# Optimization experiments

Measured on AMD Instinct MI355X. Metric: run time of the kernel, lower is better.

## Reference

```python
import jax, jax.numpy as jnp
import numpy as np

# Loss hyperparameters (from init_kwargs defaults)
ALPHA, BETA, GAMMA = 1.0, 2.0, 1.0
DAY_W, NIGHT_W = 2.0, 0.5
PEAK_WIN_W, PEAK_WIN = 3.0, 2
HIGH_POWER_W, POWER_PCT = 1.5, 0.75
HOURS = 24

B, S = 4096, 4032  # seq_len = 24 * 168 days


def setup_inputs() -> dict:
    key = jax.random.key(0)
    k1, k2 = jax.random.split(key)
    y_true = jax.random.uniform(k1, (B, S), dtype=jnp.float32)
    # predictions = truth + noise, clipped to be realistic power values
    y_pred = y_true + 0.1 * jax.random.normal(k2, (B, S), dtype=jnp.float32)
    return {"y_pred": y_pred, "y_true": y_true}


def _daily_peaks(y, day_mask):
    # y, day_mask: (B, D, H). Peaks restricted to daytime hours.
    masked = jnp.where(day_mask, y, jnp.float32(-1e9))
    times = jnp.argmax(masked, axis=-1)                                   # (B, D) int
    vals = jnp.take_along_axis(y, times[..., None], axis=-1)[..., 0]      # (B, D)
    return times, vals


def reference(y_pred, y_true):
    b, s = y_true.shape
    d = s // HOURS
    # default is_daytime: hour-of-day in [6, 20]
    hour = jnp.arange(HOURS, dtype=jnp.int32)
    day_hour_mask = (hour >= 6) & (hour <= 20)                            # (H,)
    is_daytime = jnp.broadcast_to(day_hour_mask[None, None, :], (b, d, HOURS))

    yt = y_true.reshape(b, d, HOURS)
    yp = y_pred.reshape(b, d, HOURS)

    true_times, true_peaks = _daily_peaks(yt, is_daytime)
    pred_times, pred_peaks = _daily_peaks(yp, is_daytime)
    peak_time_errors = (pred_times - true_times).astype(jnp.float32)      # (B, D)

    # --- step weights: day/night base, x PEAK_WIN_W in [peak-2, peak+2] ---
    base_w = jnp.where(is_daytime, jnp.float32(DAY_W), jnp.float32(NIGHT_W))  # (B,D,H)
    pt = true_times[..., None]                                            # (B,D,1)
    in_window = (hour[None, None, :] >= pt - PEAK_WIN) & (hour[None, None, :] <= pt + PEAK_WIN)
    step_w = base_w * jnp.where(in_window, jnp.float32(PEAK_WIN_W), jnp.float32(1.0))
    step_w = step_w.reshape(b, s)

    sq_err = (y_pred - y_true) ** 2
    L_overall = jnp.sum(sq_err * step_w) / jnp.sum(step_w)

    # --- peak magnitude loss with high-power sample weighting ---
    sample_avg_peaks = jnp.mean(true_peaks, axis=1)                       # (B,)
    thr = jnp.quantile(sample_avg_peaks, POWER_PCT)
    high = sample_avg_peaks > thr                                         # (B,) bool
    sample_w = jnp.where(high[:, None], jnp.float32(HIGH_POWER_W), jnp.float32(1.0))
    sample_w = jnp.broadcast_to(sample_w, true_peaks.shape)               # (B, D)
    peak_sq = (pred_peaks - true_peaks) ** 2
    L_peak_mag = jnp.sum(peak_sq * sample_w) / jnp.sum(sample_w)

    L_peak_timing = jnp.mean(jnp.abs(peak_time_errors) * 10.0)

    return ALPHA * L_overall + BETA * L_peak_mag + GAMMA * L_peak_timing
```

## Files before the change

kernel.cpp:

```cpp
#include <hip/hip_runtime.h>
#include <math.h>

#define S_LEN   4032
#define HOURS   24
#define DAYS    168
#define DAY_PAD 28
#define NB_MAX  4096


__device__ inline float block_reduce_f(float v, float* scratch, int tid) {
#pragma unroll
    for (int o = 32; o > 0; o >>= 1) v += __shfl_down(v, o, 64);
    if ((tid & 63) == 0) scratch[tid >> 6] = v;
    __syncthreads();
    float r = 0.f;
    if (tid == 0) r = scratch[0] + scratch[1] + scratch[2] + scratch[3];
    __syncthreads();
    return r;
}

__device__ inline double block_reduce_d(double v, double* scratch, int tid) {
#pragma unroll
    for (int o = 32; o > 0; o >>= 1) v += __shfl_down(v, o, 64);
    if ((tid & 63) == 0) scratch[tid >> 6] = v;
    __syncthreads();
    double r = 0.0;
    if (tid == 0) r = scratch[0] + scratch[1] + scratch[2] + scratch[3];
    __syncthreads();
    return r;
}


__global__ __launch_bounds__(256, 4) void day_kernel(
    const float* __restrict__ y_pred, const float* __restrict__ y_true,
    float* __restrict__ A, float* __restrict__ P,
    float* __restrict__ SEp, float* __restrict__ SWp, float* __restrict__ Tp)
{
    __shared__ float s_yt[DAYS * DAY_PAD];
    __shared__ float s_yp[DAYS * DAY_PAD];
    __shared__ float s_red[4];

    const int tid = threadIdx.x;
    const int b = blockIdx.x;
    const size_t base = (size_t)b * S_LEN;
    const float4* gp = (const float4*)(y_pred + base);
    const float4* gt = (const float4*)(y_true + base);

    for (int i = tid; i < S_LEN / 4; i += 256) {
        float4 vp = gp[i];
        float4 vt = gt[i];
        int f = i * 4;
        int d = f / HOURS;
        int off = f - d * HOURS;
        *(float4*)&s_yp[d * DAY_PAD + off] = vp;
        *(float4*)&s_yt[d * DAY_PAD + off] = vt;
    }
    __syncthreads();

    float tpeak = 0.f, psq = 0.f, se = 0.f, sw = 0.f, terr = 0.f;
    if (tid < DAYS) {
        const float4* rt = (const float4*)&s_yt[tid * DAY_PAD];
        const float4* rp = (const float4*)&s_yp[tid * DAY_PAD];
        float yt[HOURS];
#pragma unroll
        for (int j = 0; j < 6; ++j) {
            float4 q = rt[j];
            yt[j * 4 + 0] = q.x; yt[j * 4 + 1] = q.y;
            yt[j * 4 + 2] = q.z; yt[j * 4 + 3] = q.w;
        }
        float tbest = yt[6]; int tt = 6;
#pragma unroll
        for (int h = 7; h <= 20; ++h) {
            if (yt[h] > tbest) { tbest = yt[h]; tt = h; }
        }
        float pbest = -1e30f; int pt = 6;
#pragma unroll
        for (int j = 0; j < 6; ++j) {
            float4 q = rp[j];
            float pv[4] = {q.x, q.y, q.z, q.w};
#pragma unroll
            for (int k = 0; k < 4; ++k) {
                int h = j * 4 + k;
                float v = pv[k];
                bool day = (h >= 6) && (h <= 20);
                if (day && v > pbest) { pbest = v; pt = h; }
                float bw = day ? 2.0f : 0.5f;
                float w = bw * (((h >= tt - 2) && (h <= tt + 2)) ? 3.0f : 1.0f);
                float dd = v - yt[h];
                se += dd * dd * w;
                sw += w;
            }
        }
        tpeak = tbest;
        float dp = pbest - tbest;
        psq = dp * dp;
        terr = fabsf((float)(pt - tt));
    }

    float rA = block_reduce_f(tpeak, s_red, tid);
    float rP = block_reduce_f(psq,   s_red, tid);
    float rE = block_reduce_f(se,    s_red, tid);
    float rW = block_reduce_f(sw,    s_red, tid);
    float rT = block_reduce_f(terr,  s_red, tid);
    if (tid == 0) {
        A[b]   = rA * (1.0f / (float)DAYS);
        P[b]   = rP;
        SEp[b] = rE;
        SWp[b] = rW;
        Tp[b]  = rT;
    }
}


__global__ __launch_bounds__(256) void finalize_kernel(
    const float* __restrict__ A, const float* __restrict__ P,
    const float* __restrict__ SEp, const float* __restrict__ SWp,
    const float* __restrict__ Tp, float* __restrict__ out, int nB)
{
    __shared__ unsigned s_keys[NB_MAX];
    __shared__ unsigned s_hist[256];
    __shared__ unsigned s_wtot[4];
    __shared__ unsigned s_sel, s_srem;
    __shared__ double s_dred[4];

    const int tid = threadIdx.x;

    for (int i = tid; i < nB; i += 256) {
        unsigned u = __float_as_uint(A[i]);
        s_keys[i] = (u & 0x80000000u) ? ~u : (u | 0x80000000u);
    }
    __syncthreads();

    double pos = 0.75 * (double)(nB - 1);
    int lo = (int)pos;
    double frac = pos - (double)lo;
    int hi = (lo + 1 < nB) ? lo + 1 : lo;
    int ranks[2] = {lo, hi};
    float qv[2];

    for (int sidx = 0; sidx < 2; ++sidx) {
        int rem = ranks[sidx];
        unsigned prefix = 0;
        for (int shift = 24; shift >= 0; shift -= 8) {
            s_hist[tid] = 0;
            __syncthreads();
            unsigned maskAbove = (shift == 24) ? 0u : (0xFFFFFFFFu << (shift + 8));
            for (int i = tid; i < nB; i += 256) {
                unsigned k = s_keys[i];
                if ((k & maskAbove) == prefix)
                    atomicAdd(&s_hist[(k >> shift) & 0xFFu], 1u);
            }
            __syncthreads();
            unsigned c = s_hist[tid];
            unsigned x = c;
#pragma unroll
            for (int o = 1; o < 64; o <<= 1) {
                unsigned y = __shfl_up(x, o, 64);
                if ((tid & 63) >= o) x += y;
            }
            if ((tid & 63) == 63) s_wtot[tid >> 6] = x;
            __syncthreads();
            unsigned woff = 0;
            for (int w2 = 0; w2 < (tid >> 6); ++w2) woff += s_wtot[w2];
            unsigned incl = woff + x;
            unsigned excl = incl - c;
            if ((unsigned)rem >= excl && (unsigned)rem < incl) {
                s_sel = (unsigned)tid;
                s_srem = (unsigned)rem - excl;
            }
            __syncthreads();
            prefix |= (s_sel << shift);
            rem = (int)s_srem;
            __syncthreads();
        }
        unsigned bits = (prefix & 0x80000000u) ? (prefix & 0x7FFFFFFFu) : ~prefix;
        qv[sidx] = __uint_as_float(bits);
    }

    float thr = (float)((double)qv[0] + frac * ((double)qv[1] - (double)qv[0]));

    double wp = 0.0, wsum = 0.0, se = 0.0, swt = 0.0, te = 0.0;
    for (int i = tid; i < nB; i += 256) {
        float a = A[i];
        float w = (a > thr) ? 1.5f : 1.0f;
        wp   += (double)w * (double)P[i];
        wsum += (double)w;
        se   += (double)SEp[i];
        swt  += (double)SWp[i];
        te   += (double)Tp[i];
    }
    wp   = block_reduce_d(wp,   s_dred, tid);
    wsum = block_reduce_d(wsum, s_dred, tid);
    se   = block_reduce_d(se,   s_dred, tid);
    swt  = block_reduce_d(swt,  s_dred, tid);
    te   = block_reduce_d(te,   s_dred, tid);

    if (tid == 0) {
        double L_overall = se / swt;
        double L_peak    = wp / ((double)DAYS * wsum);
        double L_timing  = 10.0 * te / ((double)nB * (double)DAYS);
        out[0] = (float)(L_overall + 2.0 * L_peak + L_timing);
    }
}


extern "C" void kernel_launch(void* const* d_in, const int* in_sizes, int n_in,
                              void* d_out, int out_size, void* d_ws, size_t ws_size,
                              hipStream_t stream) {
    const float* y_pred = (const float*)d_in[0];
    const float* y_true = (const float*)d_in[1];
    int total = in_sizes[0];
    int nB = total / S_LEN;

    float* ws  = (float*)d_ws;
    float* A   = ws;
    float* P   = ws + 1 * NB_MAX;
    float* SEp = ws + 2 * NB_MAX;
    float* SWp = ws + 3 * NB_MAX;
    float* Tp  = ws + 4 * NB_MAX;

    day_kernel<<<nB, 256, 0, stream>>>(y_pred, y_true, A, P, SEp, SWp, Tp);
    finalize_kernel<<<1, 256, 0, stream>>>(A, P, SEp, SWp, Tp, (float*)d_out, nB);
}
```

Measured before the change: 175.9 us.

## Split rows into quarter-row blocks and replace radix select with parallel rank counting

The day kernel now processes 42 days per block across four blocks per row, with one thread per float4 of both inputs. It finds daily peaks through a two-level shared-memory argmax and drops the padded shared staging. The single-block radix-select quantile is replaced by a multi-block rank kernel in which each sample counts how many values are smaller or equal, and a separate finalize kernel then combines the partial sums. This raises parallelism and occupancy, at the cost of an extra launch and O(n²) comparisons for the quantile.

```diff
diff --git a/kernel.cpp b/kernel.cpp
--- a/kernel.cpp
+++ b/kernel.cpp
@@ -4,199 +4,191 @@
 #define S_LEN   4032
 #define HOURS   24
 #define DAYS    168
-#define DAY_PAD 28
+#define DPB     42
+#define ACT     252
+#define QPB     4
 #define NB_MAX  4096
 
 
-__device__ inline float block_reduce_f(float v, float* scratch, int tid) {
+__global__ __launch_bounds__(256, 8) void day_kernel(
+    const float* __restrict__ y_pred, const float* __restrict__ y_true,
+    float* __restrict__ SEp, float* __restrict__ SWp, float* __restrict__ Tp,
+    float* __restrict__ Pp, float* __restrict__ Ap)
+{
+    __shared__ float s_tv[ACT], s_pv[ACT];
+    __shared__ int   s_th[ACT], s_ph[ACT];
+    __shared__ int   s_tt[DPB];
+    __shared__ float s_red[5][4];
+
+    const int tid = threadIdx.x;
+    const int lane = tid & 63;
+    const int wv = tid >> 6;
+
+    float se = 0.f, sw = 0.f, ap = 0.f, pp = 0.f, tp = 0.f;
+
+    float yp[4], yt[4];
+    int j = tid % 6;
+    int dl = tid / 6;
+
+    if (tid < ACT) {
+        const size_t base = (size_t)blockIdx.x * (DPB * HOURS) + (size_t)tid * 4;
+        float4 p4 = *(const float4*)(y_pred + base);
+        float4 t4 = *(const float4*)(y_true + base);
+        yp[0] = p4.x; yp[1] = p4.y; yp[2] = p4.z; yp[3] = p4.w;
+        yt[0] = t4.x; yt[1] = t4.y; yt[2] = t4.z; yt[3] = t4.w;
+
+        float tv = -1e30f, pv = -1e30f; int th = 0, ph = 0;
+#pragma unroll
+        for (int k = 0; k < 4; ++k) {
+            int h = 4 * j + k;
+            bool day = (h >= 6) && (h <= 20);
+            if (day && yt[k] > tv) { tv = yt[k]; th = h; }
+            if (day && yp[k] > pv) { pv = yp[k]; ph = h; }
+        }
+        s_tv[tid] = tv; s_th[tid] = th;
+        s_pv[tid] = pv; s_ph[tid] = ph;
+    }
+    __syncthreads();
+
+    if (tid < DPB) {
+        int o = tid * 6;
+        float tb = s_tv[o]; int tt = s_th[o];
+        float pb = s_pv[o]; int pt = s_ph[o];
+#pragma unroll
+        for (int jj = 1; jj < 6; ++jj) {
+            float v = s_tv[o + jj];
+            if (v > tb) { tb = v; tt = s_th[o + jj]; }
+            float w = s_pv[o + jj];
+            if (w > pb) { pb = w; pt = s_ph[o + jj]; }
+        }
+        s_tt[tid] = tt;
+        ap = tb;
+        float dp = pb - tb;
+        pp = dp * dp;
+        tp = fabsf((float)(pt - tt));
+    }
+    __syncthreads();
+
+    if (tid < ACT) {
+        int tt = s_tt[dl];
+#pragma unroll
+        for (int k = 0; k < 4; ++k) {
+            int h = 4 * j + k;
+            bool day = (h >= 6) && (h <= 20);
+            float bw = day ? 2.0f : 0.5f;
+            float w = bw * (((h >= tt - 2) && (h <= tt + 2)) ? 3.0f : 1.0f);
+            float d = yp[k] - yt[k];
+            se = fmaf(d * d, w, se);
+            sw += w;
+        }
+    }
+
+    float vals[5] = {se, sw, ap, pp, tp};
+#pragma unroll
+    for (int q = 0; q < 5; ++q) {
+        float v = vals[q];
+#pragma unroll
+        for (int o = 32; o > 0; o >>= 1) v += __shfl_down(v, o, 64);
+        if (lane == 0) s_red[q][wv] = v;
+    }
+    __syncthreads();
+    if (tid == 0) {
+        SEp[blockIdx.x] = s_red[0][0] + s_red[0][1] + s_red[0][2] + s_red[0][3];
+        SWp[blockIdx.x] = s_red[1][0] + s_red[1][1] + s_red[1][2] + s_red[1][3];
+        Ap[blockIdx.x]  = s_red[2][0] + s_red[2][1] + s_red[2][2] + s_red[2][3];
+        Pp[blockIdx.x]  = s_red[3][0] + s_red[3][1] + s_red[3][2] + s_red[3][3];
+        Tp[blockIdx.x]  = s_red[4][0] + s_red[4][1] + s_red[4][2] + s_red[4][3];
+    }
+}
+
+
+__global__ __launch_bounds__(256) void rank_kernel(
+    const float* __restrict__ Ap, float* __restrict__ A_out,
+    float* __restrict__ qout, int nB)
+{
+    __shared__ float sA[NB_MAX];
+    const int tid = threadIdx.x;
+
+    for (int i = tid; i < nB; i += 256) {
+        float4 p = *(const float4*)(Ap + 4 * i);
+        float a = (p.x + p.y + p.z + p.w) * (1.0f / (float)DAYS);
+        sA[i] = a;
+        if (blockIdx.x == 0) A_out[i] = a;
+    }
+    __syncthreads();
+
+    const int b = blockIdx.x * 128 + (tid >> 1);
+    const int half = tid & 1;
+    if (b >= nB) return;
+    const float v = sA[b];
+    const int span = nB / 2;
+    const float4* s4 = (const float4*)(sA + half * span);
+
+    int cl = 0, ce = 0;
+    for (int i = 0; i < span / 4; ++i) {
+        float4 x = s4[i];
+        cl += (x.x < v) + (x.y < v) + (x.z < v) + (x.w < v);
+        ce += (x.x == v) + (x.y == v) + (x.z == v) + (x.w == v);
+    }
+    cl += __shfl_xor(cl, 1, 64);
+    ce += __shfl_xor(ce, 1, 64);
+
+    if (half == 0) {
+        double pos = 0.75 * (double)(nB - 1);
+        int lo = (int)pos;
+        int hi = (lo + 1 < nB) ? lo + 1 : lo;
+        if (lo >= cl && lo < cl + ce) qout[0] = v;
+        if (hi >= cl && hi < cl + ce) qout[1] = v;
+    }
+}
+
+
+__device__ inline double block_reduce_d(double v, double* scratch, int tid) {
 #pragma unroll
     for (int o = 32; o > 0; o >>= 1) v += __shfl_down(v, o, 64);
     if ((tid & 63) == 0) scratch[tid >> 6] = v;
     __syncthreads();
-    float r = 0.f;
-    if (tid == 0) r = scratch[0] + scratch[1] + scratch[2] + scratch[3];
-    __syncthreads();
-    return r;
-}
-
-__device__ inline double block_reduce_d(double v, double* scratch, int tid) {
-#pragma unroll
-    for (int o = 32; o > 0; o >>= 1) v += __shfl_down(v, o, 64);
-    if ((tid & 63) == 0) scratch[tid >> 6] = v;
-    __syncthreads();
     double r = 0.0;
     if (tid == 0) r = scratch[0] + scratch[1] + scratch[2] + scratch[3];
     __syncthreads();
     return r;
 }
 
-
-__global__ __launch_bounds__(256, 4) void day_kernel(
-    const float* __restrict__ y_pred, const float* __restrict__ y_true,
-    float* __restrict__ A, float* __restrict__ P,
-    float* __restrict__ SEp, float* __restrict__ SWp, float* __restrict__ Tp)
+__global__ __launch_bounds__(256) void final_kernel(
+    const float* __restrict__ SEp, const float* __restrict__ SWp,
+    const float* __restrict__ Tp, const float* __restrict__ Pp,
+    const float* __restrict__ A, const float* __restrict__ qout,
+    float* __restrict__ out, int nB)
 {
-    __shared__ float s_yt[DAYS * DAY_PAD];
-    __shared__ float s_yp[DAYS * DAY_PAD];
-    __shared__ float s_red[4];
-
+    __shared__ double s_dred[4];
     const int tid = threadIdx.x;
-    const int b = blockIdx.x;
-    const size_t base = (size_t)b * S_LEN;
-    const float4* gp = (const float4*)(y_pred + base);
-    const float4* gt = (const float4*)(y_true + base);
-
-    for (int i = tid; i < S_LEN / 4; i += 256) {
-        float4 vp = gp[i];
-        float4 vt = gt[i];
-        int f = i * 4;
-        int d = f / HOURS;
-        int off = f - d * HOURS;
-        *(float4*)&s_yp[d * DAY_PAD + off] = vp;
-        *(float4*)&s_yt[d * DAY_PAD + off] = vt;
-    }
-    __syncthreads();
-
-    float tpeak = 0.f, psq = 0.f, se = 0.f, sw = 0.f, terr = 0.f;
-    if (tid < DAYS) {
-        const float4* rt = (const float4*)&s_yt[tid * DAY_PAD];
-        const float4* rp = (const float4*)&s_yp[tid * DAY_PAD];
-        float yt[HOURS];
-#pragma unroll
-        for (int j = 0; j < 6; ++j) {
-            float4 q = rt[j];
-            yt[j * 4 + 0] = q.x; yt[j * 4 + 1] = q.y;
-            yt[j * 4 + 2] = q.z; yt[j * 4 + 3] = q.w;
-        }
-        float tbest = yt[6]; int tt = 6;
-#pragma unroll
-        for (int h = 7; h <= 20; ++h) {
-            if (yt[h] > tbest) { tbest = yt[h]; tt = h; }
-        }
-        float pbest = -1e30f; int pt = 6;
-#pragma unroll
-        for (int j = 0; j < 6; ++j) {
-            float4 q = rp[j];
-            float pv[4] = {q.x, q.y, q.z, q.w};
-#pragma unroll
-            for (int k = 0; k < 4; ++k) {
-                int h = j * 4 + k;
-                float v = pv[k];
-                bool day = (h >= 6) && (h <= 20);
-                if (day && v > pbest) { pbest = v; pt = h; }
-                float bw = day ? 2.0f : 0.5f;
-                float w = bw * (((h >= tt - 2) && (h <= tt + 2)) ? 3.0f : 1.0f);
-                float dd = v - yt[h];
-                se += dd * dd * w;
-                sw += w;
-            }
-        }
-        tpeak = tbest;
-        float dp = pbest - tbest;
-        psq = dp * dp;
-        terr = fabsf((float)(pt - tt));
-    }
-
-    float rA = block_reduce_f(tpeak, s_red, tid);
-    float rP = block_reduce_f(psq,   s_red, tid);
-    float rE = block_reduce_f(se,    s_red, tid);
-    float rW = block_reduce_f(sw,    s_red, tid);
-    float rT = block_reduce_f(terr,  s_red, tid);
-    if (tid == 0) {
-        A[b]   = rA * (1.0f / (float)DAYS);
-        P[b]   = rP;
-        SEp[b] = rE;
-        SWp[b] = rW;
-        Tp[b]  = rT;
-    }
-}
-
-
-__global__ __launch_bounds__(256) void finalize_kernel(
-    const float* __restrict__ A, const float* __restrict__ P,
-    const float* __restrict__ SEp, const float* __restrict__ SWp,
-    const float* __restrict__ Tp, float* __restrict__ out, int nB)
-{
-    __shared__ unsigned s_keys[NB_MAX];
-    __shared__ unsigned s_hist[256];
-    __shared__ unsigned s_wtot[4];
-    __shared__ unsigned s_sel, s_srem;
-    __shared__ double s_dred[4];
-
-    const int tid = threadIdx.x;
-
-    for (int i = tid; i < nB; i += 256) {
-        unsigned u = __float_as_uint(A[i]);
-        s_keys[i] = (u & 0x80000000u) ? ~u : (u | 0x80000000u);
-    }
-    __syncthreads();
+    const int nBlk = nB * QPB;
 
     double pos = 0.75 * (double)(nB - 1);
-    int lo = (int)pos;
-    double frac = pos - (double)lo;
-    int hi = (lo + 1 < nB) ? lo + 1 : lo;
-    int ranks[2] = {lo, hi};
-    float qv[2];
-
-    for (int sidx = 0; sidx < 2; ++sidx) {
-        int rem = ranks[sidx];
-        unsigned prefix = 0;
-        for (int shift = 24; shift >= 0; shift -= 8) {
-            s_hist[tid] = 0;
-            __syncthreads();
-            unsigned maskAbove = (shift == 24) ? 0u : (0xFFFFFFFFu << (shift + 8));
-            for (int i = tid; i < nB; i += 256) {
-                unsigned k = s_keys[i];
-                if ((k & maskAbove) == prefix)
-                    atomicAdd(&s_hist[(k >> shift) & 0xFFu], 1u);
-            }
-            __syncthreads();
-            unsigned c = s_hist[tid];
-            unsigned x = c;
-#pragma unroll
-            for (int o = 1; o < 64; o <<= 1) {
-                unsigned y = __shfl_up(x, o, 64);
-                if ((tid & 63) >= o) x += y;
-            }
-            if ((tid & 63) == 63) s_wtot[tid >> 6] = x;
-            __syncthreads();
-            unsigned woff = 0;
-            for (int w2 = 0; w2 < (tid >> 6); ++w2) woff += s_wtot[w2];
-            unsigned incl = woff + x;
-            unsigned excl = incl - c;
-            if ((unsigned)rem >= excl && (unsigned)rem < incl) {
-                s_sel = (unsigned)tid;
-                s_srem = (unsigned)rem - excl;
-            }
-            __syncthreads();
-            prefix |= (s_sel << shift);
-            rem = (int)s_srem;
-            __syncthreads();
-        }
-        unsigned bits = (prefix & 0x80000000u) ? (prefix & 0x7FFFFFFFu) : ~prefix;
-        qv[sidx] = __uint_as_float(bits);
-    }
-
-    float thr = (float)((double)qv[0] + frac * ((double)qv[1] - (double)qv[0]));
-
-    double wp = 0.0, wsum = 0.0, se = 0.0, swt = 0.0, te = 0.0;
-    for (int i = tid; i < nB; i += 256) {
-        float a = A[i];
-        float w = (a > thr) ? 1.5f : 1.0f;
-        wp   += (double)w * (double)P[i];
+    double frac = pos - (double)((int)pos);
+    float thr = (float)((double)qout[0] + frac * ((double)qout[1] - (double)qout[0]));
+
+    double se = 0.0, sw = 0.0, te = 0.0, wp = 0.0, wsum = 0.0;
+    for (int i = tid; i < nBlk; i += 256) {
+        se += (double)SEp[i];
+        sw += (double)SWp[i];
+        te += (double)Tp[i];
+    }
+    for (int b = tid; b < nB; b += 256) {
+        float4 p = *(const float4*)(Pp + 4 * b);
+        float Pb = p.x + p.y + p.z + p.w;
+        float w = (A[b] > thr) ? 1.5f : 1.0f;
+        wp   += (double)w * (double)Pb;
         wsum += (double)w;
-        se   += (double)SEp[i];
-        swt  += (double)SWp[i];
-        te   += (double)Tp[i];
-    }
+    }
+    se   = block_reduce_d(se,   s_dred, tid);
+    sw   = block_reduce_d(sw,   s_dred, tid);
+    te   = block_reduce_d(te,   s_dred, tid);
     wp   = block_reduce_d(wp,   s_dred, tid);
     wsum = block_reduce_d(wsum, s_dred, tid);
-    se   = block_reduce_d(se,   s_dred, tid);
-    swt  = block_reduce_d(swt,  s_dred, tid);
-    te   = block_reduce_d(te,   s_dred, tid);
 
     if (tid == 0) {
-        double L_overall = se / swt;
+        double L_overall = se / sw;
         double L_peak    = wp / ((double)DAYS * wsum);
         double L_timing  = 10.0 * te / ((double)nB * (double)DAYS);
         out[0] = (float)(L_overall + 2.0 * L_peak + L_timing);
@@ -211,14 +203,18 @@
     const float* y_true = (const float*)d_in[1];
     int total = in_sizes[0];
     int nB = total / S_LEN;
+    int nBlk = nB * QPB;
 
     float* ws  = (float*)d_ws;
-    float* A   = ws;
-    float* P   = ws + 1 * NB_MAX;
-    float* SEp = ws + 2 * NB_MAX;
-    float* SWp = ws + 3 * NB_MAX;
-    float* Tp  = ws + 4 * NB_MAX;
-
-    day_kernel<<<nB, 256, 0, stream>>>(y_pred, y_true, A, P, SEp, SWp, Tp);
-    finalize_kernel<<<1, 256, 0, stream>>>(A, P, SEp, SWp, Tp, (float*)d_out, nB);
-}
+    float* SEp = ws;
+    float* SWp = ws + 1 * (size_t)nBlk;
+    float* Tp  = ws + 2 * (size_t)nBlk;
+    float* Pp  = ws + 3 * (size_t)nBlk;
+    float* Ap  = ws + 4 * (size_t)nBlk;
+    float* A   = ws + 5 * (size_t)nBlk;
+    float* q   = ws + 5 * (size_t)nBlk + (size_t)nB;
+
+    day_kernel<<<nBlk, 256, 0, stream>>>(y_pred, y_true, SEp, SWp, Tp, Pp, Ap);
+    rank_kernel<<<(nB + 127) / 128, 256, 0, stream>>>(Ap, A, q, nB);
+    final_kernel<<<1, 256, 0, stream>>>(SEp, SWp, Tp, Pp, A, q, (float*)d_out, nB);
+}
```

After: 188.2 us. 1.07x slower.
